# Kernel optimization log

Hardware: AMD Instinct MI355X
Metric: run time of the kernel (lower is better)

## Reference

```python
import jax, jax.numpy as jnp
import numpy as np

N, E, D_IN, D_OUT = 16384, 4096, 256, 256


def _leaky(v):
    return jnp.where(v > 0, v, 0.1 * v)


def setup_inputs() -> dict:
    key = jax.random.key(0)
    ks = jax.random.split(key, 8)
    x = jax.random.normal(ks[0], (N, D_IN), dtype=jnp.float32)
    # 0/1 incidence mask, float32 (as multiplied in the torch code)
    H_shape = jax.random.randint(ks[1], (N, E), 0, 2).astype(jnp.float32)
    w1 = jax.random.normal(ks[2], (D_IN, D_OUT), dtype=jnp.float32)
    w2 = jax.random.normal(ks[3], (D_OUT, D_OUT), dtype=jnp.float32)
    a1 = jax.random.normal(ks[4], (D_OUT, 1), dtype=jnp.float32)
    a21 = jax.random.normal(ks[5], (D_OUT, 1), dtype=jnp.float32)
    a22 = jax.random.normal(ks[6], (D_OUT, 1), dtype=jnp.float32)
    return {"x": x, "H_shape": H_shape, "w1": w1, "w2": w2,
            "a1": a1, "a21": a21, "a22": a22}


def reference(x, H_shape, w1, w2, a1, a21, a22):
    xw1 = x @ w1                                  # [N, D]
    # node->edge attention (masked softmax-like over nodes, axis -2)
    f = _leaky(xw1) @ a1                          # [N, 1]
    e = jnp.exp(jnp.tanh(f / 8) * 8) * H_shape    # [N, E]
    e = e / jnp.sum(e, axis=-2, keepdims=True)    # normalize over nodes
    # edge features
    f = _leaky(e.T @ xw1)                         # [E, D]
    # edge->node attention (masked normalize over edges, axis -1)
    b = (_leaky(f @ w2) @ a21).T + _leaky(xw1) @ a22  # [1,E] + [N,1] -> [N,E]
    b = jnp.exp(jnp.tanh(b / 8) * 8) * H_shape
    b = b / jnp.sum(b, axis=-1, keepdims=True)
    return _leaky(b @ f @ w2)                     # [N, D]
```

## Files before the change

kernel.cpp:

```cpp
#include <hip/hip_runtime.h>


typedef __attribute__((ext_vector_type(8))) short short8;
typedef __attribute__((ext_vector_type(4))) short short4v;
typedef __attribute__((ext_vector_type(4))) float f32x4;
typedef __attribute__((ext_vector_type(4))) int int4v;
typedef __attribute__((ext_vector_type(4))) unsigned int uint4v;

__device__ __forceinline__ float leakyf(float v) { return v > 0.f ? v : 0.1f * v; }
__device__ __forceinline__ float fastrcp(float x) { return __builtin_amdgcn_rcpf(x); }

__device__ __forceinline__ float satexpf(float t) {
    float u = fminf(fmaxf(t * 0.25f, -30.f), 30.f);
    float p = __expf(u);
    float th = (p - 1.f) * fastrcp(p + 1.f);
    return __expf(8.f * th);
}

__device__ __forceinline__ short f2b(float v) {
    unsigned int x = __float_as_uint(v);
    x += 0x7fffu + ((x >> 16) & 1u);
    return (short)(x >> 16);
}
__device__ __forceinline__ float b2f(short s) {
    return __uint_as_float(((unsigned int)(unsigned short)s) << 16);
}
__device__ __forceinline__ unsigned int bits4_to_bytes(unsigned int s) {
    return ((s & 0xFu) * 0x00204081u) & 0x01010101u;
}

__global__ __launch_bounds__(256) void transposeH_pack(
        const float* __restrict__ H, unsigned int* __restrict__ Hbits,
        unsigned int* __restrict__ HbitsT, unsigned int* __restrict__ ddmax,
        float* __restrict__ cat,
        const float* __restrict__ w1, short* __restrict__ w1Th, short* __restrict__ w1Tl,
        const float* __restrict__ w2, short* __restrict__ w2Th, short* __restrict__ w2Tl) {
    __shared__ float Ts[64][65];
    const int t = threadIdx.x;
    const long r0 = (long)blockIdx.x * 64;
    const long c0 = (long)blockIdx.y * 64;
    if (blockIdx.x == 0 && blockIdx.y == 0) {
        if (t < 256) ddmax[t] = 0u;
        if (t < 32) ddmax[256 + t] = 0u;
#pragma unroll
        for (int i = 0; i < 16; ++i) cat[t * 16 + i] = 0.f;
    }
    if (blockIdx.x < 4 && blockIdx.y < 8) {
        const int zz = blockIdx.y >> 2;
        const float* src = zz ? w2 : w1;
        short* dh = zz ? w2Th : w1Th;
        short* dl = zz ? w2Tl : w1Tl;
        const long sr0 = (long)blockIdx.x * 64;
        const long sc0 = (long)(blockIdx.y & 3) * 64;
        {
            const int row = t >> 2, cc = (t & 3) * 16;
            const float* p = src + (sr0 + row) * 256 + sc0 + cc;
#pragma unroll
            for (int i = 0; i < 4; ++i) {
                f32x4 v = *reinterpret_cast<const f32x4*>(p + i * 4);
#pragma unroll
                for (int k = 0; k < 4; ++k) Ts[row][cc + i * 4 + k] = v[k];
            }
        }
        __syncthreads();
        {
            const int cl = t >> 2, ch = (t & 3) * 16;
            short8 h0, h1, l0, l1;
#pragma unroll
            for (int i = 0; i < 8; ++i) {
                float v = Ts[ch + i][cl];
                short h = f2b(v);
                h0[i] = h; l0[i] = f2b(v - b2f(h));
            }
#pragma unroll
            for (int i = 0; i < 8; ++i) {
                float v = Ts[ch + 8 + i][cl];
                short h = f2b(v);
                h1[i] = h; l1[i] = f2b(v - b2f(h));
            }
            short* qh = dh + (sc0 + cl) * 256 + sr0 + ch;
            short* ql = dl + (sc0 + cl) * 256 + sr0 + ch;
            *reinterpret_cast<short8*>(qh) = h0;
            *reinterpret_cast<short8*>(qh + 8) = h1;
            *reinterpret_cast<short8*>(ql) = l0;
            *reinterpret_cast<short8*>(ql + 8) = l1;
        }
        __syncthreads();
    }
    {
        const int row = t >> 2, cc = (t & 3) * 16;
        const float* p = H + (r0 + row) * 4096L + c0 + cc;
#pragma unroll
        for (int i = 0; i < 4; ++i) {
            f32x4 v = *reinterpret_cast<const f32x4*>(p + i * 4);
#pragma unroll
            for (int k = 0; k < 4; ++k) Ts[row][cc + i * 4 + k] = v[k];
        }
    }
    __syncthreads();
    if (t < 128) {
        const int nl = t >> 1, w = t & 1;
        unsigned int u = 0;
#pragma unroll
        for (int b = 0; b < 32; ++b)
            u |= (Ts[nl][w * 32 + b] != 0.f ? 1u : 0u) << b;
        Hbits[(r0 + nl) * 128 + (c0 >> 5) + w] = u;
    } else {
        const int t2 = t - 128;
        const int jl = t2 >> 1, w = t2 & 1;
        unsigned int u = 0;
#pragma unroll
        for (int b = 0; b < 32; ++b)
            u |= (Ts[w * 32 + b][jl] != 0.f ? 1u : 0u) << b;
        HbitsT[(c0 + jl) * 512 + (r0 >> 5) + w] = u;
    }
}

__global__ __launch_bounds__(256) void gemm_xw1(
        const float* __restrict__ A, const short* __restrict__ Bh,
        const short* __restrict__ Bl, float* __restrict__ C) {
    __shared__ short Ash[128][72];
    __shared__ short Asl[128][72];
    __shared__ short Bsh[64][72];
    __shared__ short Bsl[64][72];
    const int t = threadIdx.x;
    const int wid = t >> 6, lane = t & 63;
    const int wm = wid & 1, wn = wid >> 1;
    const int quad = lane >> 4, l15 = lane & 15;
    const long m0 = (long)blockIdx.x * 128;
    const long n0 = (long)blockIdx.y * 64;
    int rA[4], cA[4], rB[2], cB[2];
#pragma unroll
    for (int it = 0; it < 4; ++it) {
        const int cid = t + it * 256;
        rA[it] = cid >> 3; cA[it] = (cid & 7) * 8;
    }
#pragma unroll
    for (int it = 0; it < 2; ++it) {
        const int cid = t + it * 256;
        rB[it] = cid >> 3; cB[it] = (cid & 7) * 8;
    }
    f32x4 acc[4][2];
#pragma unroll
    for (int i = 0; i < 4; ++i)
#pragma unroll
        for (int j = 0; j < 2; ++j)
#pragma unroll
            for (int r = 0; r < 4; ++r) acc[i][j][r] = 0.f;

    f32x4 av0[4], av1[4];
    short8 bvh[2], bvl[2];
#pragma unroll
    for (int it = 0; it < 4; ++it) {
        const float* ap = A + (m0 + rA[it]) * 256 + cA[it];
        av0[it] = *reinterpret_cast<const f32x4*>(ap);
        av1[it] = *reinterpret_cast<const f32x4*>(ap + 4);
    }
#pragma unroll
    for (int it = 0; it < 2; ++it) {
        bvh[it] = *reinterpret_cast<const short8*>(Bh + (n0 + rB[it]) * 256 + cB[it]);
        bvl[it] = *reinterpret_cast<const short8*>(Bl + (n0 + rB[it]) * 256 + cB[it]);
    }

    for (int kb = 0; kb < 256; kb += 64) {
#pragma unroll
        for (int it = 0; it < 4; ++it) {
            short8 hi, lo;
#pragma unroll
            for (int k = 0; k < 4; ++k) {
                short h0 = f2b(av0[it][k]); hi[k] = h0; lo[k] = f2b(av0[it][k] - b2f(h0));
                short h1 = f2b(av1[it][k]); hi[4 + k] = h1; lo[4 + k] = f2b(av1[it][k] - b2f(h1));
            }
            *reinterpret_cast<short8*>(&Ash[rA[it]][cA[it]]) = hi;
            *reinterpret_cast<short8*>(&Asl[rA[it]][cA[it]]) = lo;
        }
#pragma unroll
        for (int it = 0; it < 2; ++it) {
            *reinterpret_cast<short8*>(&Bsh[rB[it]][cB[it]]) = bvh[it];
            *reinterpret_cast<short8*>(&Bsl[rB[it]][cB[it]]) = bvl[it];
        }
        __syncthreads();
        const bool pf = (kb < 192);
        f32x4 an0[4], an1[4];
        short8 bnh[2], bnl[2];
        if (pf) {
#pragma unroll
            for (int it = 0; it < 4; ++it) {
                const float* ap = A + (m0 + rA[it]) * 256 + kb + 64 + cA[it];
                an0[it] = *reinterpret_cast<const f32x4*>(ap);
                an1[it] = *reinterpret_cast<const f32x4*>(ap + 4);
            }
#pragma unroll
            for (int it = 0; it < 2; ++it) {
                bnh[it] = *reinterpret_cast<const short8*>(Bh + (n0 + rB[it]) * 256 + kb + 64 + cB[it]);
                bnl[it] = *reinterpret_cast<const short8*>(Bl + (n0 + rB[it]) * 256 + kb + 64 + cB[it]);
            }
        }
#pragma unroll
        for (int ks = 0; ks < 2; ++ks) {
            short8 ah[4], al[4], bh[2], bl[2];
#pragma unroll
            for (int i = 0; i < 4; ++i) {
                ah[i] = *reinterpret_cast<const short8*>(&Ash[wm * 64 + i * 16 + l15][ks * 32 + quad * 8]);
                al[i] = *reinterpret_cast<const short8*>(&Asl[wm * 64 + i * 16 + l15][ks * 32 + quad * 8]);
            }
#pragma unroll
            for (int j = 0; j < 2; ++j) {
                bh[j] = *reinterpret_cast<const short8*>(&Bsh[wn * 32 + j * 16 + l15][ks * 32 + quad * 8]);
                bl[j] = *reinterpret_cast<const short8*>(&Bsl[wn * 32 + j * 16 + l15][ks * 32 + quad * 8]);
            }
#pragma unroll
            for (int i = 0; i < 4; ++i)
#pragma unroll
                for (int j = 0; j < 2; ++j) {
                    acc[i][j] = __builtin_amdgcn_mfma_f32_16x16x32_bf16(ah[i], bh[j], acc[i][j], 0, 0, 0);
                    acc[i][j] = __builtin_amdgcn_mfma_f32_16x16x32_bf16(ah[i], bl[j], acc[i][j], 0, 0, 0);
                    acc[i][j] = __builtin_amdgcn_mfma_f32_16x16x32_bf16(al[i], bh[j], acc[i][j], 0, 0, 0);
                }
        }
        __syncthreads();
        if (pf) {
#pragma unroll
            for (int it = 0; it < 4; ++it) { av0[it] = an0[it]; av1[it] = an1[it]; }
#pragma unroll
            for (int it = 0; it < 2; ++it) { bvh[it] = bnh[it]; bvl[it] = bnl[it]; }
        }
    }
#pragma unroll
    for (int i = 0; i < 4; ++i) {
        const long grow = m0 + wm * 64 + i * 16 + quad * 4;
#pragma unroll
        for (int j = 0; j < 2; ++j) {
            const long gcol = n0 + wn * 32 + j * 16 + l15;
#pragma unroll
            for (int r = 0; r < 4; ++r)
                C[(grow + r) * 256 + gcol] = acc[i][j][r];
        }
    }
}

__global__ __launch_bounds__(256) void node_stats1(
        const float* __restrict__ xw1, const float* __restrict__ a1,
        const float* __restrict__ a22, float* __restrict__ g_out,
        float* __restrict__ dn, unsigned int* __restrict__ ddmax) {
    __shared__ float Mx[4][260];
    const int t = threadIdx.x;
    const int n0 = blockIdx.x * 64;
    const int r = t >> 2, q = t & 3;
    const long n = n0 + r;
    const float* xp = xw1 + n * 256 + q * 64;
    float vals[64];
    float facc = 0.f, dacc = 0.f;
#pragma unroll
    for (int i = 0; i < 16; ++i) {
        f32x4 v  = *reinterpret_cast<const f32x4*>(xp + i * 4);
        f32x4 b1 = *reinterpret_cast<const f32x4*>(a1 + q * 64 + i * 4);
        f32x4 b2 = *reinterpret_cast<const f32x4*>(a22 + q * 64 + i * 4);
#pragma unroll
        for (int k = 0; k < 4; ++k) {
            float lv = leakyf(v[k]);
            facc += lv * b1[k];
            dacc += lv * b2[k];
            vals[i * 4 + k] = v[k];
        }
    }
    facc += __shfl_xor(facc, 1); facc += __shfl_xor(facc, 2);
    dacc += __shfl_xor(dacc, 1); dacc += __shfl_xor(dacc, 2);
    const float g = satexpf(facc);
    if (q == 0) { dn[n] = dacc; g_out[n] = g; }
    float lm[64];
#pragma unroll
    for (int i = 0; i < 64; ++i) lm[i] = fabsf(vals[i] * g);
#pragma unroll
    for (int m = 4; m < 64; m <<= 1)
#pragma unroll
        for (int i = 0; i < 64; ++i) lm[i] = fmaxf(lm[i], __shfl_xor(lm[i], m));
    float gm = g;
#pragma unroll
    for (int m = 1; m < 64; m <<= 1) gm = fmaxf(gm, __shfl_xor(gm, m));
    const int wv = t >> 6, lane = t & 63;
    if (lane < 4) {
#pragma unroll
        for (int i = 0; i < 64; ++i) Mx[wv][lane * 64 + i] = lm[i];
    }
    if (lane == 0) Mx[wv][256] = gm;
    __syncthreads();
    if (t < 256) {
        float m = fmaxf(fmaxf(Mx[0][t], Mx[1][t]), fmaxf(Mx[2][t], Mx[3][t]));
        atomicMax(&ddmax[t], __float_as_uint(m));
    }
    if (t == 0) {
        float m = fmaxf(fmaxf(Mx[0][256], Mx[1][256]), fmaxf(Mx[2][256], Mx[3][256]));
        atomicMax(&ddmax[256], __float_as_uint(m));
    }
}

__global__ __launch_bounds__(256) void quantize_y(
        const float* __restrict__ xw1, const float* __restrict__ g_in,
        const unsigned int* __restrict__ ddmax, char* __restrict__ yQ) {
    __shared__ unsigned int Qh[257][16];
    __shared__ unsigned int Ql[257][16];
    const int t = threadIdx.x;
    const int n0 = blockIdx.x * 64;
    const int dd0 = (t >> 4) * 16;
    const int w = t & 15;
    const int r4 = w * 4;
    float s[16];
#pragma unroll
    for (int i = 0; i < 16; ++i)
        s[i] = 32512.f / __uint_as_float(ddmax[dd0 + i]);
    const float sg = 32512.f / __uint_as_float(ddmax[256]);
    unsigned int bh[16], bl[16];
#pragma unroll
    for (int i = 0; i < 16; ++i) { bh[i] = 0u; bl[i] = 0u; }
    unsigned int gh = 0u, gl = 0u;
#pragma unroll
    for (int rr = 0; rr < 4; ++rr) {
        const long n = n0 + r4 + rr;
        const float gg = g_in[n];
        const float* xp = xw1 + n * 256 + dd0;
#pragma unroll
        for (int c = 0; c < 4; ++c) {
            f32x4 v = *reinterpret_cast<const f32x4*>(xp + c * 4);
#pragma unroll
            for (int k = 0; k < 4; ++k) {
                const int i = c * 4 + k;
                int qv = __float2int_rn(v[k] * gg * s[i]);
                qv = max(-32639, min(32639, qv));
                const int qh = (qv + 128) >> 8;
                const int ql = qv - (qh << 8);
                bh[i] |= ((unsigned int)(qh & 255)) << (8 * rr);
                bl[i] |= ((unsigned int)(ql & 255)) << (8 * rr);
            }
        }
        if (t < 16) {
            int qv = __float2int_rn(gg * sg);
            qv = max(-32639, min(32639, qv));
            const int qh = (qv + 128) >> 8;
            const int ql = qv - (qh << 8);
            gh |= ((unsigned int)(qh & 255)) << (8 * rr);
            gl |= ((unsigned int)(ql & 255)) << (8 * rr);
        }
    }
#pragma unroll
    for (int i = 0; i < 16; ++i) { Qh[dd0 + i][w] = bh[i]; Ql[dd0 + i][w] = bl[i]; }
    if (t < 16) { Qh[256][t] = gh; Ql[256][t] = gl; }
    __syncthreads();
#pragma unroll
    for (int it = 0; it < 2; ++it) {
        const int dd = it * 256 + t;
        if (dd < 288) {
#pragma unroll
            for (int s2 = 0; s2 < 4; ++s2) {
                uint4v vh, vl;
                if (dd < 257) {
                    vh = *reinterpret_cast<const uint4v*>(&Qh[dd][s2 * 4]);
                    vl = *reinterpret_cast<const uint4v*>(&Ql[dd][s2 * 4]);
                } else {
#pragma unroll
                    for (int k = 0; k < 4; ++k) { vh[k] = 0u; vl[k] = 0u; }
                }
                *reinterpret_cast<uint4v*>(yQ + (long)dd * 16384 + n0 + s2 * 16) = vh;
                *reinterpret_cast<uint4v*>(yQ + (long)(288 + dd) * 16384 + n0 + s2 * 16) = vl;
            }
        }
    }
}

__global__ __launch_bounds__(256) void gemm_c1_bits(
        const unsigned int* __restrict__ HbitsT, const char* __restrict__ Bb,
        float* __restrict__ Cp) {
    __shared__ char Bsh[48][144];
    __shared__ char Bsl[48][144];
    const int t = threadIdx.x;
    const int wid = t >> 6, lane = t & 63;
    const int quad = lane >> 4, l15 = lane & 15;
    const long m0 = (long)blockIdx.x * 256;
    const long n0 = (long)blockIdx.y * 48;
    const long k0 = (long)blockIdx.z * 2048;
    float* Cz = Cp + (long)blockIdx.z * (4096L * 288);
    const unsigned int* bp[4];
#pragma unroll
    for (int i = 0; i < 4; ++i)
        bp[i] = HbitsT + (m0 + wid * 64 + i * 16 + l15) * 512 + (k0 >> 5);
    char* dstp[3];
    long sbase[3];
#pragma unroll
    for (int it = 0; it < 3; ++it) {
        const int cid = t + it * 256;
        const int idx = (cid < 384) ? cid : cid - 384;
        const int row = idx >> 3, seg = (idx & 7) * 16;
        dstp[it] = (cid >= 384) ? &Bsl[row][seg] : &Bsh[row][seg];
        const long srow = (cid >= 384) ? (288 + n0 + row) : (n0 + row);
        sbase[it] = srow * 16384 + k0 + seg;
    }
    int4v acch[4][3], accl[4][3];
#pragma unroll
    for (int i = 0; i < 4; ++i)
#pragma unroll
        for (int j = 0; j < 3; ++j)
#pragma unroll
            for (int r = 0; r < 4; ++r) { acch[i][j][r] = 0; accl[i][j][r] = 0; }

    uint4v bv[4], sv[3];
#pragma unroll
    for (int i = 0; i < 4; ++i)
        bv[i] = *reinterpret_cast<const uint4v*>(bp[i]);
#pragma unroll
    for (int it = 0; it < 3; ++it)
        sv[it] = *reinterpret_cast<const uint4v*>(Bb + sbase[it]);

    for (int kb = 0; kb < 2048; kb += 128) {
#pragma unroll
        for (int it = 0; it < 3; ++it)
            *reinterpret_cast<uint4v*>(dstp[it]) = sv[it];
        __syncthreads();
        const bool pf = (kb < 1920);
        uint4v bvn[4], svn[3];
        if (pf) {
#pragma unroll
            for (int i = 0; i < 4; ++i)
                bvn[i] = *reinterpret_cast<const uint4v*>(bp[i] + ((kb + 128) >> 5));
#pragma unroll
            for (int it = 0; it < 3; ++it)
                svn[it] = *reinterpret_cast<const uint4v*>(Bb + sbase[it] + kb + 128);
        }
#pragma unroll
        for (int ks = 0; ks < 2; ++ks) {
            int4v af[4], bh[3], bl[3];
#pragma unroll
            for (int i = 0; i < 4; ++i) {
                const unsigned int u =
                    bv[i][ks * 2 + (quad >> 1)] >> ((quad & 1) * 16);
                uint4v e;
#pragma unroll
                for (int k = 0; k < 4; ++k) e[k] = bits4_to_bytes(u >> (4 * k));
                af[i] = __builtin_bit_cast(int4v, e);
            }
#pragma unroll
            for (int j = 0; j < 3; ++j) {
                bh[j] = *reinterpret_cast<const int4v*>(&Bsh[j * 16 + l15][ks * 64 + quad * 16]);
                bl[j] = *reinterpret_cast<const int4v*>(&Bsl[j * 16 + l15][ks * 64 + quad * 16]);
            }
#pragma unroll
            for (int i = 0; i < 4; ++i)
#pragma unroll
                for (int j = 0; j < 3; ++j) {
                    acch[i][j] = __builtin_amdgcn_mfma_i32_16x16x64_i8(af[i], bh[j], acch[i][j], 0, 0, 0);
                    accl[i][j] = __builtin_amdgcn_mfma_i32_16x16x64_i8(af[i], bl[j], accl[i][j], 0, 0, 0);
                }
        }
        __syncthreads();
        if (pf) {
#pragma unroll
            for (int i = 0; i < 4; ++i) bv[i] = bvn[i];
#pragma unroll
            for (int it = 0; it < 3; ++it) sv[it] = svn[it];
        }
    }
#pragma unroll
    for (int i = 0; i < 4; ++i) {
        const long grow = m0 + wid * 64 + i * 16 + quad * 4;
#pragma unroll
        for (int j = 0; j < 3; ++j) {
            const long gcol = n0 + j * 16 + l15;
#pragma unroll
            for (int r = 0; r < 4; ++r)
                Cz[(grow + r) * 288 + gcol] =
                    256.f * (float)acch[i][j][r] + (float)accl[i][j][r];
        }
    }
}

__global__ __launch_bounds__(256) void reduce_C1(
        const float* __restrict__ C1p, const unsigned int* __restrict__ ddmax,
        float* __restrict__ C1) {
    const int i = blockIdx.x * 256 + threadIdx.x;
    const int dd = i % 288;
    float s = 0.f;
#pragma unroll
    for (int z = 0; z < 8; ++z) s += C1p[(long)z * 4096 * 288 + i];
    C1[i] = s * (__uint_as_float(ddmax[dd]) * (1.f / 32512.f));
}

__global__ __launch_bounds__(256) void gemm_G(
        const float* __restrict__ C1, const short* __restrict__ w2Th,
        const short* __restrict__ w2Tl, const float* __restrict__ a21,
        short* __restrict__ GT, float* __restrict__ cat) {
    __shared__ short Ash[64][72];
    __shared__ short Asl[64][72];
    __shared__ short Bsh[64][72];
    __shared__ short Bsl[64][72];
    __shared__ float Gs[64][65];
    const int t = threadIdx.x;
    const int wid = t >> 6, lane = t & 63;
    const int wm = wid & 1, wn = wid >> 1;
    const int quad = lane >> 4, l15 = lane & 15;
    const long j0 = (long)blockIdx.x * 64;
    const long d0 = (long)blockIdx.y * 64;
    int rS[2], cS[2];
#pragma unroll
    for (int it = 0; it < 2; ++it) {
        const int cid = t + it * 256;
        rS[it] = cid >> 3; cS[it] = (cid & 7) * 8;
    }
    f32x4 acc[2][2];
#pragma unroll
    for (int i = 0; i < 2; ++i)
#pragma unroll
        for (int j = 0; j < 2; ++j)
#pragma unroll
            for (int r = 0; r < 4; ++r) acc[i][j][r] = 0.f;

    float rdv[2];
    f32x4 av0[2], av1[2];
    short8 bvh[2], bvl[2];
#pragma unroll
    for (int it = 0; it < 2; ++it) {
        rdv[it] = fastrcp(C1[(j0 + rS[it]) * 288 + 256]);
        const float* ap = C1 + (j0 + rS[it]) * 288 + cS[it];
        av0[it] = *reinterpret_cast<const f32x4*>(ap);
        av1[it] = *reinterpret_cast<const f32x4*>(ap + 4);
        bvh[it] = *reinterpret_cast<const short8*>(w2Th + (d0 + rS[it]) * 256 + cS[it]);
        bvl[it] = *reinterpret_cast<const short8*>(w2Tl + (d0 + rS[it]) * 256 + cS[it]);
    }

    for (int kb = 0; kb < 256; kb += 64) {
#pragma unroll
        for (int it = 0; it < 2; ++it) {
            short8 hi, lo;
#pragma unroll
            for (int k = 0; k < 4; ++k) {
                float f0 = leakyf(av0[it][k] * rdv[it]);
                float f1 = leakyf(av1[it][k] * rdv[it]);
                short h0 = f2b(f0); hi[k] = h0; lo[k] = f2b(f0 - b2f(h0));
                short h1 = f2b(f1); hi[4 + k] = h1; lo[4 + k] = f2b(f1 - b2f(h1));
            }
            *reinterpret_cast<short8*>(&Ash[rS[it]][cS[it]]) = hi;
            *reinterpret_cast<short8*>(&Asl[rS[it]][cS[it]]) = lo;
            *reinterpret_cast<short8*>(&Bsh[rS[it]][cS[it]]) = bvh[it];
            *reinterpret_cast<short8*>(&Bsl[rS[it]][cS[it]]) = bvl[it];
        }
        __syncthreads();
        const bool pf = (kb < 192);
        f32x4 an0[2], an1[2];
        short8 bnh[2], bnl[2];
        if (pf) {
#pragma unroll
            for (int it = 0; it < 2; ++it) {
                const float* ap = C1 + (j0 + rS[it]) * 288 + kb + 64 + cS[it];
                an0[it] = *reinterpret_cast<const f32x4*>(ap);
                an1[it] = *reinterpret_cast<const f32x4*>(ap + 4);
                bnh[it] = *reinterpret_cast<const short8*>(w2Th + (d0 + rS[it]) * 256 + kb + 64 + cS[it]);
                bnl[it] = *reinterpret_cast<const short8*>(w2Tl + (d0 + rS[it]) * 256 + kb + 64 + cS[it]);
            }
        }
#pragma unroll
        for (int ks = 0; ks < 2; ++ks) {
            short8 ah[2], al[2], bh[2], bl[2];
#pragma unroll
            for (int i = 0; i < 2; ++i) {
                ah[i] = *reinterpret_cast<const short8*>(&Ash[wm * 32 + i * 16 + l15][ks * 32 + quad * 8]);
                al[i] = *reinterpret_cast<const short8*>(&Asl[wm * 32 + i * 16 + l15][ks * 32 + quad * 8]);
            }
#pragma unroll
            for (int j = 0; j < 2; ++j) {
                bh[j] = *reinterpret_cast<const short8*>(&Bsh[wn * 32 + j * 16 + l15][ks * 32 + quad * 8]);
                bl[j] = *reinterpret_cast<const short8*>(&Bsl[wn * 32 + j * 16 + l15][ks * 32 + quad * 8]);
            }
#pragma unroll
            for (int i = 0; i < 2; ++i)
#pragma unroll
                for (int j = 0; j < 2; ++j) {
                    acc[i][j] = __builtin_amdgcn_mfma_f32_16x16x32_bf16(ah[i], bh[j], acc[i][j], 0, 0, 0);
                    acc[i][j] = __builtin_amdgcn_mfma_f32_16x16x32_bf16(ah[i], bl[j], acc[i][j], 0, 0, 0);
                    acc[i][j] = __builtin_amdgcn_mfma_f32_16x16x32_bf16(al[i], bh[j], acc[i][j], 0, 0, 0);
                }
        }
        __syncthreads();
        if (pf) {
#pragma unroll
            for (int it = 0; it < 2; ++it) {
                av0[it] = an0[it]; av1[it] = an1[it];
                bvh[it] = bnh[it]; bvl[it] = bnl[it];
            }
        }
    }
#pragma unroll
    for (int i = 0; i < 2; ++i)
#pragma unroll
        for (int j = 0; j < 2; ++j)
#pragma unroll
            for (int r = 0; r < 4; ++r)
                Gs[wm * 32 + i * 16 + quad * 4 + r][wn * 32 + j * 16 + l15] = acc[i][j][r];
    __syncthreads();
    {
        const int jl = t >> 2, q = t & 3;
        float cp = 0.f;
#pragma unroll
        for (int i = 0; i < 16; ++i) {
            const int d = q * 16 + i;
            cp += leakyf(Gs[jl][d]) * a21[d0 + d];
        }
        cp += __shfl_xor(cp, 1); cp += __shfl_xor(cp, 2);
        if (q == 0) atomicAdd(&cat[j0 + jl], cp);
    }
    {
        const int dl = t >> 2, q = t & 3;
        short8 pk0, pk1;
#pragma unroll
        for (int i = 0; i < 8; ++i) pk0[i] = f2b(Gs[q * 16 + i][dl]);
#pragma unroll
        for (int i = 0; i < 8; ++i) pk1[i] = f2b(Gs[q * 16 + 8 + i][dl]);
        short* gp = GT + (d0 + dl) * 4096 + j0 + q * 16;
        *reinterpret_cast<short8*>(gp) = pk0;
        *reinterpret_cast<short8*>(gp + 8) = pk1;
    }
}

__global__ __launch_bounds__(512, 4) void fused_out_split(
        const unsigned int* __restrict__ Hbits, const float* __restrict__ cat,
        const float* __restrict__ dn, const short* __restrict__ GT,
        float* __restrict__ outP, float* __restrict__ rsP) {
    __shared__ short As[64][72];
    __shared__ short Bs[256][72];
    __shared__ float rsS[64][8];
    const int t = threadIdx.x;
    const int wid = t >> 6, lane = t & 63;
    const int wm = wid >> 2, wn = wid & 3;
    const int quad = lane >> 4, l15 = lane & 15;
    const long m0 = (long)blockIdx.x * 64;
    const int z = blockIdx.y;
    const int kbase = z * 2048;
    const int r = t & 63, c8 = t >> 6;
    const float drow = dn[m0 + r];
    const int bo = (c8 & 3) * 8;

    f32x4 acc[2][4];
#pragma unroll
    for (int i = 0; i < 2; ++i)
#pragma unroll
        for (int j = 0; j < 4; ++j)
#pragma unroll
            for (int x = 0; x < 4; ++x) acc[i][j][x] = 0.f;
    float racc = 0.f;

    short8 gv[4];
    short8 pkc;
    {
        const int kb = kbase;
#pragma unroll
        for (int it = 0; it < 4; ++it) {
            const int cid = t + it * 512;
            const int row = cid >> 3, cc = (cid & 7) * 8;
            gv[it] = *reinterpret_cast<const short8*>(GT + row * 4096 + kb + cc);
        }
        const unsigned int w = Hbits[(m0 + r) * 128 + (kb >> 5) + (c8 >> 2)];
        const f32x4 cv0 = *reinterpret_cast<const f32x4*>(cat + kb + c8 * 8);
        const f32x4 cv1 = *reinterpret_cast<const f32x4*>(cat + kb + c8 * 8 + 4);
#pragma unroll
        for (int k = 0; k < 8; ++k) {
            const float cvk = (k < 4) ? cv0[k & 3] : cv1[k & 3];
            const float s = ((w >> (bo + k)) & 1u) ? satexpf(cvk + drow) : 0.f;
            const short sb = f2b(s);
            pkc[k] = sb;
            racc += b2f(sb);
        }
    }

    for (int kk = 0; kk < 2048; kk += 64) {
        const int kb = kbase + kk;
#pragma unroll
        for (int it = 0; it < 4; ++it) {
            const int cid = t + it * 512;
            const int row = cid >> 3, cc = (cid & 7) * 8;
            *reinterpret_cast<short8*>(&Bs[row][cc]) = gv[it];
        }
        *reinterpret_cast<short8*>(&As[r][c8 * 8]) = pkc;
        __syncthreads();

        const bool pf = (kk < 1984);
        unsigned int hw = 0u;
        f32x4 cn0{}, cn1{};
        if (pf) {
            const int kn = kb + 64;
#pragma unroll
            for (int it = 0; it < 4; ++it) {
                const int cid = t + it * 512;
                const int row = cid >> 3, cc = (cid & 7) * 8;
                gv[it] = *reinterpret_cast<const short8*>(GT + row * 4096 + kn + cc);
            }
            hw = Hbits[(m0 + r) * 128 + (kn >> 5) + (c8 >> 2)];
            cn0 = *reinterpret_cast<const f32x4*>(cat + kn + c8 * 8);
            cn1 = *reinterpret_cast<const f32x4*>(cat + kn + c8 * 8 + 4);
        }

#pragma unroll
        for (int ks = 0; ks < 2; ++ks) {
            short8 af[2], bf[4];
#pragma unroll
            for (int i = 0; i < 2; ++i)
                af[i] = *reinterpret_cast<const short8*>(
                        &As[wm * 32 + i * 16 + l15][ks * 32 + quad * 8]);
#pragma unroll
            for (int j = 0; j < 4; ++j)
                bf[j] = *reinterpret_cast<const short8*>(
                        &Bs[wn * 64 + j * 16 + l15][ks * 32 + quad * 8]);
#pragma unroll
            for (int i = 0; i < 2; ++i)
#pragma unroll
                for (int j = 0; j < 4; ++j)
                    acc[i][j] = __builtin_amdgcn_mfma_f32_16x16x32_bf16(
                            af[i], bf[j], acc[i][j], 0, 0, 0);
        }

        if (pf) {
#pragma unroll
            for (int k = 0; k < 8; ++k) {
                const float cvk = (k < 4) ? cn0[k & 3] : cn1[k & 3];
                const float s = ((hw >> (bo + k)) & 1u) ? satexpf(cvk + drow) : 0.f;
                const short sb = f2b(s);
                pkc[k] = sb;
                racc += b2f(sb);
            }
        }
        __syncthreads();
    }
    rsS[r][c8] = racc;
    __syncthreads();
    if (t < 64) {
        float s = 0.f;
#pragma unroll
        for (int i = 0; i < 8; ++i) s += rsS[t][i];
        rsP[z * 16384 + m0 + t] = s;
    }
    float* op = outP + (long)z * (16384L * 256);
#pragma unroll
    for (int i = 0; i < 2; ++i) {
#pragma unroll
        for (int j = 0; j < 4; ++j) {
            const long gcol = wn * 64 + j * 16 + l15;
#pragma unroll
            for (int x = 0; x < 4; ++x) {
                const long grow = m0 + wm * 32 + i * 16 + quad * 4 + x;
                op[grow * 256 + gcol] = acc[i][j][x];
            }
        }
    }
}

__global__ __launch_bounds__(256) void combine_out(
        const float* __restrict__ outP, const float* __restrict__ rsP,
        float* __restrict__ out) {
    const long i = ((long)blockIdx.x * 256 + threadIdx.x) * 4;
    const long n = i >> 8;
    f32x4 s = *reinterpret_cast<const f32x4*>(outP + i);
    {
        f32x4 v = *reinterpret_cast<const f32x4*>(outP + (16384L * 256) + i);
#pragma unroll
        for (int k = 0; k < 4; ++k) s[k] += v[k];
    }
    const float rinv = fastrcp(rsP[n] + rsP[16384 + n]);
    f32x4 o;
#pragma unroll
    for (int k = 0; k < 4; ++k) o[k] = leakyf(s[k] * rinv);
    *reinterpret_cast<f32x4*>(out + i) = o;
}

extern "C" void kernel_launch(void* const* d_in, const int* in_sizes, int n_in,
                              void* d_out, int out_size, void* d_ws, size_t ws_size,
                              hipStream_t stream) {
    const float* x   = (const float*)d_in[0];
    const float* H   = (const float*)d_in[1];
    const float* w1  = (const float*)d_in[2];
    const float* w2  = (const float*)d_in[3];
    const float* a1  = (const float*)d_in[4];
    const float* a21 = (const float*)d_in[5];
    const float* a22 = (const float*)d_in[6];
    float* out = (float*)d_out;
    char* ws = (char*)d_ws;

    float* xw1   = (float*)(ws + 0);
    float* C1p   = (float*)(ws + 0);
    char*  yQ    = (char*)(ws + 67108864);
    float* dn    = (float*)(ws + 76546048);
    float* g     = (float*)(ws + 76611584);
    unsigned int* ddmax = (unsigned int*)(ws + 76677120);
    short* w1Th  = (short*)(ws + 76681216);
    short* w1Tl  = (short*)(ws + 76812288);
    short* w2Th  = (short*)(ws + 76943360);
    short* w2Tl  = (short*)(ws + 77074432);
    float* C1    = (float*)(ws + 77205504);
    short* GT    = (short*)(ws + 81924096);
    float* cat   = (float*)(ws + 84021248);
    unsigned int* Hbits  = (unsigned int*)(ws + 84037632);
    unsigned int* HbitsT = (unsigned int*)(ws + 92426240);
    float* outP  = (float*)(ws + 134217728);
    float* rsP   = (float*)(ws + 201326592);

    transposeH_pack<<<dim3(256, 64), 256, 0, stream>>>(
            H, Hbits, HbitsT, ddmax, cat, w1, w1Th, w1Tl, w2, w2Th, w2Tl);

    gemm_xw1<<<dim3(128, 4), 256, 0, stream>>>(x, w1Th, w1Tl, xw1);
    node_stats1<<<dim3(256), 256, 0, stream>>>(xw1, a1, a22, g, dn, ddmax);
    quantize_y<<<dim3(256), 256, 0, stream>>>(xw1, g, ddmax, yQ);

    gemm_c1_bits<<<dim3(16, 6, 8), 256, 0, stream>>>(HbitsT, yQ, C1p);
    reduce_C1<<<dim3(4608), 256, 0, stream>>>(C1p, ddmax, C1);

    gemm_G<<<dim3(64, 4), 256, 0, stream>>>(C1, w2Th, w2Tl, a21, GT, cat);

    fused_out_split<<<dim3(256, 2), 512, 0, stream>>>(Hbits, cat, dn, GT, outP, rsP);
    combine_out<<<dim3(4096), 256, 0, stream>>>(outP, rsP, out);
}
```

Baseline: 587.6 us.

## Fold split-K reductions into producer kernels via last-block atomic counters

Removes the separate reduce_C1 and combine_out kernels. Each split-K tile now increments an atomic counter, and the last-arriving block sums the partials and writes the final result with scaling or leaky activation. This saves two kernel launches and lets the reduction overlap with other blocks' GEMM work. In exchange it adds threadfences and atomics, and the tail reduction work is serialized onto a few blocks.

```diff
diff --git a/kernel.cpp b/kernel.cpp
--- a/kernel.cpp
+++ b/kernel.cpp
@@ -34,7 +34,8 @@
         unsigned int* __restrict__ HbitsT, unsigned int* __restrict__ ddmax,
         float* __restrict__ cat,
         const float* __restrict__ w1, short* __restrict__ w1Th, short* __restrict__ w1Tl,
-        const float* __restrict__ w2, short* __restrict__ w2Th, short* __restrict__ w2Tl) {
+        const float* __restrict__ w2, short* __restrict__ w2Th, short* __restrict__ w2Tl,
+        unsigned int* __restrict__ cntC1, unsigned int* __restrict__ cntF) {
     __shared__ float Ts[64][65];
     const int t = threadIdx.x;
     const long r0 = (long)blockIdx.x * 64;
@@ -44,6 +45,8 @@
         if (t < 32) ddmax[256 + t] = 0u;
 #pragma unroll
         for (int i = 0; i < 16; ++i) cat[t * 16 + i] = 0.f;
+        if (t < 96) cntC1[t] = 0u;
+        cntF[t] = 0u;
     }
     if (blockIdx.x < 4 && blockIdx.y < 8) {
         const int zz = blockIdx.y >> 2;
@@ -369,9 +372,11 @@
 
 __global__ __launch_bounds__(256) void gemm_c1_bits(
         const unsigned int* __restrict__ HbitsT, const char* __restrict__ Bb,
-        float* __restrict__ Cp) {
+        float* __restrict__ Cp, const unsigned int* __restrict__ ddmax,
+        float* __restrict__ C1, unsigned int* __restrict__ cntC1) {
     __shared__ char Bsh[48][144];
     __shared__ char Bsl[48][144];
+    __shared__ unsigned int lastz;
     const int t = threadIdx.x;
     const int wid = t >> 6, lane = t & 63;
     const int quad = lane >> 4, l15 = lane & 15;
@@ -470,17 +475,32 @@
                     256.f * (float)acch[i][j][r] + (float)accl[i][j][r];
         }
     }
-}
-
-__global__ __launch_bounds__(256) void reduce_C1(
-        const float* __restrict__ C1p, const unsigned int* __restrict__ ddmax,
-        float* __restrict__ C1) {
-    const int i = blockIdx.x * 256 + threadIdx.x;
-    const int dd = i % 288;
-    float s = 0.f;
-#pragma unroll
-    for (int z = 0; z < 8; ++z) s += C1p[(long)z * 4096 * 288 + i];
-    C1[i] = s * (__uint_as_float(ddmax[dd]) * (1.f / 32512.f));
+    __threadfence();
+    if (t == 0) lastz = atomicAdd(&cntC1[blockIdx.y * 16 + blockIdx.x], 1u);
+    __syncthreads();
+    if (lastz == 7) {
+        __threadfence();
+        const long row = m0 + t;
+#pragma unroll
+        for (int c4 = 0; c4 < 12; ++c4) {
+            const long col = n0 + c4 * 4;
+            f32x4 s;
+#pragma unroll
+            for (int k = 0; k < 4; ++k) s[k] = 0.f;
+#pragma unroll
+            for (int z = 0; z < 8; ++z) {
+                f32x4 v = *reinterpret_cast<const f32x4*>(
+                        &Cp[(long)z * (4096L * 288) + row * 288 + col]);
+#pragma unroll
+                for (int k = 0; k < 4; ++k) s[k] += v[k];
+            }
+            f32x4 o;
+#pragma unroll
+            for (int k = 0; k < 4; ++k)
+                o[k] = s[k] * (__uint_as_float(ddmax[col + k]) * (1.f / 32512.f));
+            *reinterpret_cast<f32x4*>(&C1[row * 288 + col]) = o;
+        }
+    }
 }
 
 __global__ __launch_bounds__(256) void gemm_G(
@@ -621,10 +641,12 @@
 __global__ __launch_bounds__(512, 4) void fused_out_split(
         const unsigned int* __restrict__ Hbits, const float* __restrict__ cat,
         const float* __restrict__ dn, const short* __restrict__ GT,
-        float* __restrict__ outP, float* __restrict__ rsP) {
+        float* __restrict__ outP, float* __restrict__ rsP,
+        float* __restrict__ out, unsigned int* __restrict__ cntF) {
     __shared__ short As[64][72];
     __shared__ short Bs[256][72];
     __shared__ float rsS[64][8];
+    __shared__ unsigned int lastf;
     const int t = threadIdx.x;
     const int wid = t >> 6, lane = t & 63;
     const int wm = wid >> 2, wn = wid & 3;
@@ -747,24 +769,27 @@
             }
         }
     }
-}
-
-__global__ __launch_bounds__(256) void combine_out(
-        const float* __restrict__ outP, const float* __restrict__ rsP,
-        float* __restrict__ out) {
-    const long i = ((long)blockIdx.x * 256 + threadIdx.x) * 4;
-    const long n = i >> 8;
-    f32x4 s = *reinterpret_cast<const f32x4*>(outP + i);
-    {
-        f32x4 v = *reinterpret_cast<const f32x4*>(outP + (16384L * 256) + i);
-#pragma unroll
-        for (int k = 0; k < 4; ++k) s[k] += v[k];
-    }
-    const float rinv = fastrcp(rsP[n] + rsP[16384 + n]);
-    f32x4 o;
-#pragma unroll
-    for (int k = 0; k < 4; ++k) o[k] = leakyf(s[k] * rinv);
-    *reinterpret_cast<f32x4*>(out + i) = o;
+    __threadfence();
+    if (t == 0) lastf = atomicAdd(&cntF[blockIdx.x], 1u);
+    __syncthreads();
+    if (lastf == 1) {
+        __threadfence();
+        const long base = m0 * 256;
+#pragma unroll
+        for (int it = 0; it < 8; ++it) {
+            const long i = base + t * 4 + (long)it * 2048;
+            const long n = i >> 8;
+            f32x4 s = *reinterpret_cast<const f32x4*>(&outP[i]);
+            f32x4 v = *reinterpret_cast<const f32x4*>(&outP[16384L * 256 + i]);
+#pragma unroll
+            for (int k = 0; k < 4; ++k) s[k] += v[k];
+            const float rinv = fastrcp(rsP[n] + rsP[16384 + n]);
+            f32x4 o;
+#pragma unroll
+            for (int k = 0; k < 4; ++k) o[k] = leakyf(s[k] * rinv);
+            *reinterpret_cast<f32x4*>(&out[i]) = o;
+        }
+    }
 }
 
 extern "C" void kernel_launch(void* const* d_in, const int* in_sizes, int n_in,
@@ -797,19 +822,21 @@
     unsigned int* HbitsT = (unsigned int*)(ws + 92426240);
     float* outP  = (float*)(ws + 134217728);
     float* rsP   = (float*)(ws + 201326592);
+    unsigned int* cntC1 = (unsigned int*)(ws + 201457664);
+    unsigned int* cntF  = (unsigned int*)(ws + 201458176);
 
     transposeH_pack<<<dim3(256, 64), 256, 0, stream>>>(
-            H, Hbits, HbitsT, ddmax, cat, w1, w1Th, w1Tl, w2, w2Th, w2Tl);
+            H, Hbits, HbitsT, ddmax, cat, w1, w1Th, w1Tl, w2, w2Th, w2Tl,
+            cntC1, cntF);
 
     gemm_xw1<<<dim3(128, 4), 256, 0, stream>>>(x, w1Th, w1Tl, xw1);
     node_stats1<<<dim3(256), 256, 0, stream>>>(xw1, a1, a22, g, dn, ddmax);
     quantize_y<<<dim3(256), 256, 0, stream>>>(xw1, g, ddmax, yQ);
 
-    gemm_c1_bits<<<dim3(16, 6, 8), 256, 0, stream>>>(HbitsT, yQ, C1p);
-    reduce_C1<<<dim3(4608), 256, 0, stream>>>(C1p, ddmax, C1);
+    gemm_c1_bits<<<dim3(16, 6, 8), 256, 0, stream>>>(HbitsT, yQ, C1p, ddmax, C1, cntC1);
 
     gemm_G<<<dim3(64, 4), 256, 0, stream>>>(C1, w2Th, w2Tl, a21, GT, cat);
 
-    fused_out_split<<<dim3(256, 2), 512, 0, stream>>>(Hbits, cat, dn, GT, outP, rsP);
-    combine_out<<<dim3(4096), 256, 0, stream>>>(outP, rsP, out);
-}
+    fused_out_split<<<dim3(256, 2), 512, 0, stream>>>(
+            Hbits, cat, dn, GT, outP, rsP, out, cntF);
+}
```

Result: slower. 887.3 us (+51.0%).
